# Performance work log

Measured on AMD Instinct MI355X. Metric: run time of the kernel, lower is better.

The kernel has to match this reference:

```python
import jax, jax.numpy as jnp
import numpy as np

D_HEAD = 64
MASK_FILL = -1000000.0


def setup_inputs() -> dict:
    key = jax.random.key(0)
    ks = jax.random.split(key, 5)
    batch, seq, d_model, n_heads, d_head = 4, 2048, 1024, 16, D_HEAD
    # xavier_uniform bound for [d_model, n_heads, d_head]: treated as fan_in=d_model, fan_out=n_heads*d_head
    bound_qkv = float(np.sqrt(6.0 / (d_model + n_heads * d_head)))
    bound_out = float(np.sqrt(6.0 / (d_head + n_heads * d_model)))
    return {
        "resid": jax.random.normal(ks[0], (batch, seq, d_model), dtype=jnp.float32),
        "W_Q": jax.random.uniform(ks[1], (d_model, n_heads, d_head), jnp.float32, -bound_qkv, bound_qkv),
        "W_K": jax.random.uniform(ks[2], (d_model, n_heads, d_head), jnp.float32, -bound_qkv, bound_qkv),
        "W_V": jax.random.uniform(ks[3], (d_model, n_heads, d_head), jnp.float32, -bound_qkv, bound_qkv),
        "W_out": jax.random.uniform(ks[4], (d_head, n_heads, d_model), jnp.float32, -bound_out, bound_out),
        "b_out": jnp.zeros((d_model,), dtype=jnp.float32),
    }


def reference(resid, W_Q, W_K, W_V, W_out, b_out):
    # resid: [b, s, d]; W_Q/K/V: [d, h, dh]; W_out: [dh, h, d]
    seq = resid.shape[1]
    d_head = W_Q.shape[-1]
    q = jnp.einsum('bsd,dhk->bshk', resid, W_Q)
    k = jnp.einsum('bsd,dhk->bshk', resid, W_K)
    v = jnp.einsum('bsd,dhk->bshk', resid, W_V)
    scores = jnp.einsum('bqhk,bkhd->bhqd', q, k.astype(q.dtype)) if False else jnp.einsum('bqhc,bshc->bhqs', q, k)
    scores = scores / jnp.sqrt(jnp.asarray(d_head, dtype=scores.dtype))
    causal_mask = jnp.triu(jnp.ones((seq, seq), dtype=bool), k=1)
    scores = jnp.where(causal_mask, MASK_FILL, scores)
    probs = jax.nn.softmax(scores, axis=-1)  # [b, h, q, s]
    z = jnp.einsum('bhqs,bshc->bqhc', probs, v)
    out = jnp.einsum('bqhc,chd->bqd', z, W_out) + b_out
    return out
```

## Files before the change

### kernel.cpp

```cpp
#include <hip/hip_runtime.h>
#include <hip/hip_bf16.h>


typedef short s16x8 __attribute__((ext_vector_type(8)));
typedef short s16x4 __attribute__((ext_vector_type(4)));
typedef float f32x4 __attribute__((ext_vector_type(4)));

#define MFMA_BF16(A, B, C) __builtin_amdgcn_mfma_f32_16x16x32_bf16((A), (B), (C), 0, 0, 0)

#if __has_builtin(__builtin_amdgcn_exp2f)
#define EXP2(x) __builtin_amdgcn_exp2f(x)
#else
#define EXP2(x) exp2f(x)
#endif
#if __has_builtin(__builtin_amdgcn_rcpf)
#define RCP(x) __builtin_amdgcn_rcpf(x)
#else
#define RCP(x) (1.0f / (x))
#endif

__device__ __forceinline__ short f2bf(float f) {
    __bf16 h = (__bf16)f;
    return __builtin_bit_cast(short, h);
}

__device__ __forceinline__ void gld16(const unsigned short* g, unsigned short* l) {
    __builtin_amdgcn_global_load_lds(
        (const __attribute__((address_space(1))) unsigned int*)g,
        (__attribute__((address_space(3))) unsigned int*)l, 16, 0, 0);
}

__global__ __launch_bounds__(256) void prep_fused(
    const float* __restrict__ resid, const float* __restrict__ WQ,
    const float* __restrict__ WK, const float* __restrict__ WV,
    const float* __restrict__ Wout,
    unsigned short* __restrict__ residb, unsigned short* __restrict__ Wqkvt,
    unsigned short* __restrict__ W2t)
{
    const int bid = blockIdx.x;
    if (bid < 8192) {
        const int i = bid * 256 + threadIdx.x;
        const float4 v = ((const float4*)resid)[i];
        s16x4 o;
        o[0] = f2bf(v.x); o[1] = f2bf(v.y); o[2] = f2bf(v.z); o[3] = f2bf(v.w);
        *(s16x4*)(residb + (size_t)i * 4) = o;
        return;
    }
    __shared__ unsigned short tile[64][66];
    const int id2 = bid - 8192;
    const int which = id2 >> 8;
    const int sub = id2 & 255;
    const int tx = threadIdx.x & 63, ty = threadIdx.x >> 6;
    if (which < 3) {
        const float* W = which == 0 ? WQ : (which == 1 ? WK : WV);
        unsigned short* Wt = Wqkvt + (size_t)which * 1024 * 1024;
        const int n0 = (sub & 15) * 64, k0 = (sub >> 4) * 64;
        #pragma unroll
        for (int i = ty; i < 64; i += 4)
            tile[i][tx] = (unsigned short)f2bf(W[(size_t)(k0 + i) * 1024 + n0 + tx]);
        __syncthreads();
        #pragma unroll
        for (int i = ty; i < 64; i += 4)
            Wt[(size_t)(n0 + i) * 1024 + k0 + tx] = tile[tx][i];
    } else {
        const int d0 = (sub & 15) * 64, h = sub >> 4;
        #pragma unroll
        for (int c = ty; c < 64; c += 4)
            tile[c][tx] = (unsigned short)f2bf(Wout[(size_t)(c * 16 + h) * 1024 + d0 + tx]);
        __syncthreads();
        #pragma unroll
        for (int i = ty; i < 64; i += 4)
            W2t[(size_t)(d0 + i) * 1024 + h * 64 + tx] = tile[tx][i];
    }
}

template <int MODE>
__global__ __launch_bounds__(256, 2) void gemm_bt(
    const unsigned short* __restrict__ A,
    const unsigned short* __restrict__ Bt,
    float* __restrict__ Cf, const float* __restrict__ bias,
    unsigned short* __restrict__ Qb, unsigned short* __restrict__ Kb,
    unsigned short* __restrict__ Vt,
    int M, int N, int K)
{
    __shared__ __align__(16) unsigned short AB[2 * 128 * 72];
    const int tid  = threadIdx.x;
    const int lane = tid & 63;
    const int w    = tid >> 6;
    const int wm   = w & 1, wn = w >> 1;
    const int quad = lane >> 4, fl = lane & 15;
    const int m0 = blockIdx.y * 128, n0 = blockIdx.x * 128;

    const unsigned short* gp[9];
    unsigned ldso[9];
    #pragma unroll
    for (int i = 0; i < 9; ++i) {
        const int c = i * 256 + tid;
        const int cm = c % 1152;
        const int r = cm / 9, cl0 = cm % 9;
        const int cl = (cl0 == 8) ? 0 : cl0;
        gp[i] = (c < 1152 ? A + (size_t)(m0 + r) * K : Bt + (size_t)(n0 + r) * K) + cl * 8;
        ldso[i] = (unsigned)c * 8u;
    }

    f32x4 acc[4][4];
    #pragma unroll
    for (int i = 0; i < 4; ++i)
        #pragma unroll
        for (int j = 0; j < 4; ++j)
            acc[i][j] = (f32x4){0.f, 0.f, 0.f, 0.f};

    for (int kt = 0; kt < K; kt += 64) {
        __syncthreads();
        #pragma unroll
        for (int i = 0; i < 9; ++i)
            gld16(gp[i] + kt, AB + ldso[i]);
        __syncthreads();
        #pragma unroll
        for (int ko = 0; ko < 2; ++ko) {
            s16x8 af[4], bf[4];
            #pragma unroll
            for (int mi = 0; mi < 4; ++mi)
                af[mi] = *(const s16x8*)(AB + (wm * 64 + mi * 16 + fl) * 72 + ko * 32 + quad * 8);
            #pragma unroll
            for (int ni = 0; ni < 4; ++ni)
                bf[ni] = *(const s16x8*)(AB + 9216 + (wn * 64 + ni * 16 + fl) * 72 + ko * 32 + quad * 8);
            #pragma unroll
            for (int mi = 0; mi < 4; ++mi)
                #pragma unroll
                for (int ni = 0; ni < 4; ++ni)
                    acc[mi][ni] = MFMA_BF16(af[mi], bf[ni], acc[mi][ni]);
        }
    }

    if (MODE == 0) {
        #pragma unroll
        for (int ni = 0; ni < 4; ++ni) {
            const int col = n0 + wn * 64 + ni * 16 + fl;
            const float bv = bias[col];
            #pragma unroll
            for (int mi = 0; mi < 4; ++mi) {
                const int row = m0 + wm * 64 + mi * 16 + quad * 4;
                #pragma unroll
                for (int r = 0; r < 4; ++r)
                    Cf[(size_t)(row + r) * N + col] = acc[mi][ni][r] + bv;
            }
        }
    } else {
        #pragma unroll
        for (int ni = 0; ni < 4; ++ni) {
            const int colg = n0 + wn * 64 + ni * 16 + fl;
            #pragma unroll
            for (int mi = 0; mi < 4; ++mi) {
                const int token = m0 + wm * 64 + mi * 16 + quad * 4;
                if (n0 < 1024) {
                    #pragma unroll
                    for (int r = 0; r < 4; ++r)
                        Qb[(size_t)(token + r) * 1024 + colg] = (unsigned short)f2bf(acc[mi][ni][r]);
                } else if (n0 < 2048) {
                    #pragma unroll
                    for (int r = 0; r < 4; ++r)
                        Kb[(size_t)(token + r) * 1024 + (colg - 1024)] = (unsigned short)f2bf(acc[mi][ni][r]);
                } else {
                    const int cc = colg - 2048;
                    const int hh = cc >> 6, cl = cc & 63;
                    const int bb = token >> 11, ss = token & 2047;
                    s16x4 pv;
                    pv[0] = f2bf(acc[mi][ni][0]); pv[1] = f2bf(acc[mi][ni][1]);
                    pv[2] = f2bf(acc[mi][ni][2]); pv[3] = f2bf(acc[mi][ni][3]);
                    *(s16x4*)(Vt + (size_t)((bb * 16 + hh) * 64 + cl) * 2048 + ss) = pv;
                }
            }
        }
    }
}

template <bool DIAG>
__device__ __forceinline__ void attn_tile(
    int s0, int wl, int wq0, int fl, int quad,
    const unsigned short* __restrict__ KV, const unsigned short* __restrict__ Vs,
    unsigned short* __restrict__ PbW,
    const s16x8 (&qfr)[2][2], f32x4 (&zt)[2][4], float (&ls)[2])
{
    const float SC = 0.18033688011112042f;
    const float M  = 32.0f;
    #pragma unroll
    for (int c4 = 0; c4 < 4; ++c4) {
        if (DIAG && c4 > wl) break;
        #pragma unroll
        for (int e = 0; e < 2; ++e) {
            const int f = 2 * c4 + e;
            const unsigned short* Krow = KV + (f * 16 + fl) * 72;
            const s16x8 kf0 = *(const s16x8*)(Krow + quad * 8);
            const s16x8 kf1 = *(const s16x8*)(Krow + 32 + quad * 8);
            #pragma unroll
            for (int g = 0; g < 2; ++g) {
                unsigned short* pw = PbW + (g * 16 + fl) * 36 + e * 16 + quad * 4;
                if (DIAG && f > 2 * wl + g) {
                    *(s16x4*)pw = (s16x4){0, 0, 0, 0};
                } else {
                    f32x4 z = (f32x4){0.f, 0.f, 0.f, 0.f};
                    z = MFMA_BF16(kf0, qfr[g][0], z);
                    z = MFMA_BF16(kf1, qfr[g][1], z);
                    float p[4];
                    #pragma unroll
                    for (int r = 0; r < 4; ++r) {
                        float arg = fmaf(z[r], SC, -M);
                        if (DIAG && f == 2 * wl + g) {
                            const int s = s0 + f * 16 + quad * 4 + r;
                            const int qi = wq0 + g * 16 + fl;
                            if (s > qi) arg = -100.f;
                        }
                        p[r] = EXP2(arg);
                    }
                    ls[g] += (p[0] + p[1]) + (p[2] + p[3]);
                    s16x4 pk;
                    pk[0] = f2bf(p[0]); pk[1] = f2bf(p[1]);
                    pk[2] = f2bf(p[2]); pk[3] = f2bf(p[3]);
                    *(s16x4*)pw = pk;
                }
            }
        }
        const s16x8 pf0 = *(const s16x8*)(PbW + fl * 36 + quad * 8);
        const s16x8 pf1 = *(const s16x8*)(PbW + (16 + fl) * 36 + quad * 8);
        #pragma unroll
        for (int mf = 0; mf < 4; ++mf) {
            const s16x8 vf = *(const s16x8*)(Vs + (mf * 16 + fl) * 136 + c4 * 32 + quad * 8);
            zt[0][mf] = MFMA_BF16(vf, pf0, zt[0][mf]);
            zt[1][mf] = MFMA_BF16(vf, pf1, zt[1][mf]);
        }
    }
}

__global__ __launch_bounds__(512, 4) void attn_causal(
    const unsigned short* __restrict__ Qb,
    const unsigned short* __restrict__ Kb,
    const unsigned short* __restrict__ Vt,
    unsigned short* __restrict__ Zb)
{
    __shared__ __align__(16) unsigned short KV[17920];
    __shared__ __align__(16) unsigned short Pb[8][32 * 36];
    const int tid = threadIdx.x, lane = tid & 63, w = tid >> 6;
    const int quad = lane >> 4, fl = lane & 15;
    const int lid = blockIdx.x;
    const int g8 = lid >> 6;
    const int qb = g8 < 4 ? 7 - g8 : g8 - 4;
    const int bh = lid & 63, b = bh >> 4, h = bh & 15;
    const int wq0 = qb * 256 + w * 32;
    const int wl = w & 3;
    const int dt = 2 * qb + (w >> 2);

    const unsigned short* Kbase = Kb + (size_t)b * 2048 * 1024 + h * 64;
    const unsigned short* Vbase = Vt + (size_t)bh * 64 * 2048;
    unsigned short* PbW = Pb[w];
    const unsigned short* Vs = KV + 9216;

    s16x8 qfr[2][2];
    #pragma unroll
    for (int g = 0; g < 2; ++g) {
        const unsigned short* Qrow = Qb + (size_t)(b * 2048 + wq0 + g * 16 + fl) * 1024 + h * 64;
        qfr[g][0] = *(const s16x8*)(Qrow + quad * 8);
        qfr[g][1] = *(const s16x8*)(Qrow + 32 + quad * 8);
    }

    const unsigned short* gsp[5];
    int sadv[5];
    unsigned ldsb[5];
    #pragma unroll
    for (int i = 0; i < 5; ++i) {
        const int W = w + 8 * i;
        if (W < 35) {
            const int c = W * 64 + lane;
            if (c < 1152) {
                const int r = c / 9, cl0 = c % 9;
                const int cl = (cl0 == 8) ? 0 : cl0;
                gsp[i] = Kbase + r * 1024 + cl * 8;  sadv[i] = 128 * 1024;
            } else {
                const int cc = c - 1152;
                const int r = cc / 17, cl0 = cc % 17;
                const int cl = (cl0 == 16) ? 0 : cl0;
                gsp[i] = Vbase + r * 2048 + cl * 8;  sadv[i] = 128;
            }
            ldsb[i] = (unsigned)c * 8u;
        }
    }

    f32x4 zt[2][4];
    #pragma unroll
    for (int g = 0; g < 2; ++g)
        #pragma unroll
        for (int mf = 0; mf < 4; ++mf) zt[g][mf] = (f32x4){0.f, 0.f, 0.f, 0.f};
    float ls[2] = {0.f, 0.f};
    const int ntiles = 2 * qb + 2;

    for (int kt = 0; kt < ntiles; ++kt) {
        __syncthreads();
        #pragma unroll
        for (int i = 0; i < 5; ++i)
            if (w + 8 * i < 35)
                gld16(gsp[i], KV + ldsb[i]);
        #pragma unroll
        for (int i = 0; i < 5; ++i)
            if (w + 8 * i < 35)
                gsp[i] += sadv[i];
        __syncthreads();

        if (kt < dt) {
            attn_tile<false>(kt << 7, wl, wq0, fl, quad, KV, Vs, PbW, qfr, zt, ls);
        } else if (kt == dt) {
            attn_tile<true>(kt << 7, wl, wq0, fl, quad, KV, Vs, PbW, qfr, zt, ls);
        }
    }
    #pragma unroll
    for (int g = 0; g < 2; ++g) {
        float lt = ls[g];
        lt += __shfl_xor(lt, 16);
        lt += __shfl_xor(lt, 32);
        const float inv = RCP(lt);
        unsigned short* Zrow = Zb + (size_t)(b * 2048 + wq0 + g * 16 + fl) * 1024 + h * 64;
        #pragma unroll
        for (int mf = 0; mf < 4; ++mf) {
            s16x4 o;
            o[0] = f2bf(zt[g][mf][0] * inv); o[1] = f2bf(zt[g][mf][1] * inv);
            o[2] = f2bf(zt[g][mf][2] * inv); o[3] = f2bf(zt[g][mf][3] * inv);
            *(s16x4*)(Zrow + mf * 16 + quad * 4) = o;
        }
    }
}

extern "C" void kernel_launch(void* const* d_in, const int* in_sizes, int n_in,
                              void* d_out, int out_size, void* d_ws, size_t ws_size,
                              hipStream_t stream) {
    const float* resid = (const float*)d_in[0];
    const float* WQ    = (const float*)d_in[1];
    const float* WK    = (const float*)d_in[2];
    const float* WV    = (const float*)d_in[3];
    const float* Wout  = (const float*)d_in[4];
    const float* bout  = (const float*)d_in[5];
    float* out = (float*)d_out;

    char* p = (char*)d_ws;
    auto alloc = [&](size_t bytes) { void* r = (void*)p; p += (bytes + 255) & ~(size_t)255; return r; };
    unsigned short* residb = (unsigned short*)alloc(8192ull * 1024 * 2);
    unsigned short* Wqkvt  = (unsigned short*)alloc(3072ull * 1024 * 2);
    unsigned short* W2t    = (unsigned short*)alloc(1024ull * 1024 * 2);
    unsigned short* Qbuf   = (unsigned short*)alloc(8192ull * 1024 * 2);
    unsigned short* Kbuf   = (unsigned short*)alloc(8192ull * 1024 * 2);
    unsigned short* Vtb    = (unsigned short*)alloc(64ull * 64 * 2048 * 2);
    unsigned short* Zbuf   = (unsigned short*)alloc(8192ull * 1024 * 2);

    prep_fused<<<9216, 256, 0, stream>>>(resid, WQ, WK, WV, Wout, residb, Wqkvt, W2t);
    gemm_bt<1><<<dim3(24, 64), 256, 0, stream>>>(residb, Wqkvt, nullptr, nullptr,
                                                 Qbuf, Kbuf, Vtb, 8192, 3072, 1024);
    attn_causal<<<512, 512, 0, stream>>>(Qbuf, Kbuf, Vtb, Zbuf);
    gemm_bt<0><<<dim3(8, 64), 256, 0, stream>>>(Zbuf, W2t, out, bout,
                                                nullptr, nullptr, nullptr, 8192, 1024, 1024);
}
```

Baseline: 261.5 us.

## Replace QKV projection GEMM with 256x256-tile, 8-wave pipelined kernel

Adds a dedicated QKV projection kernel using 256x256 output tiles with 512 threads, double-buffered 128 KB dynamic LDS loaded through direct global-to-LDS copies, XOR-swizzled layout, a grouped block-index swizzle for L2 locality, and interleaved barriers with raised priority around MFMA phases. The aim is more data reuse per loaded tile and better overlap of loads with matrix math than the previous 128-tile GEMM. In exchange it uses far more LDS per block, which limits occupancy, and it hardcodes the problem shape.

```diff
diff --git a/kernel.cpp b/kernel.cpp
--- a/kernel.cpp
+++ b/kernel.cpp
@@ -71,6 +71,161 @@
         #pragma unroll
         for (int i = ty; i < 64; i += 4)
             W2t[(size_t)(d0 + i) * 1024 + h * 64 + tx] = tile[tx][i];
+    }
+}
+
+__global__ __launch_bounds__(512, 2) void gemm256_qkv(
+    const unsigned short* __restrict__ A,
+    const unsigned short* __restrict__ Bt,
+    unsigned short* __restrict__ Qb, unsigned short* __restrict__ Kb,
+    unsigned short* __restrict__ Vt)
+{
+    extern __shared__ __align__(16) unsigned short S[];
+    constexpr int LDK = 1024, NT = 16;
+    const int tid = threadIdx.x, lane = tid & 63, w = tid >> 6;
+    const int wm = w >> 2, wn = w & 3;
+    const int quad = lane >> 4, fl = lane & 15;
+
+    const int wg  = blockIdx.x;
+    const int swz = (wg & 7) * 48 + (wg >> 3);
+    const int bx  = swz % 12, by = swz / 12;
+    const int m0  = by * 256, n0 = bx * 256;
+
+    const int srow = (tid >> 6) * 16 + (lane >> 2);
+    const int sswz = ((lane & 3) ^ ((lane >> 2) & 3)) * 8;
+    const unsigned short* pa[2];
+    const unsigned short* pb[2];
+    #pragma unroll
+    for (int j = 0; j < 2; ++j) {
+        pa[j] = A  + (size_t)(m0 + srow + j * 128) * LDK + sswz;
+        pb[j] = Bt + (size_t)(n0 + srow + j * 128) * LDK + sswz;
+    }
+    const int dst = tid * 8;
+
+    const int sxor = (quad ^ (fl & 3)) * 8;
+    const int aoff = (wm * 128 + fl) * 32 + sxor;
+    const int boff = 16384 + (wn * 64 + fl) * 32 + sxor;
+
+    f32x4 acc[8][4];
+    #pragma unroll
+    for (int m = 0; m < 8; ++m)
+        #pragma unroll
+        for (int n = 0; n < 4; ++n) acc[m][n] = (f32x4){0.f, 0.f, 0.f, 0.f};
+
+    gld16(pa[0], S + dst);
+    gld16(pa[1], S + 4096 + dst);
+    gld16(pb[0], S + 16384 + dst);
+    gld16(pb[1], S + 20480 + dst);
+    gld16(pa[0] + 32, S + 8192 + dst);
+    gld16(pa[1] + 32, S + 12288 + dst);
+    gld16(pb[0] + 32, S + 24576 + dst);
+    gld16(pb[1] + 32, S + 28672 + dst);
+
+    for (int t = 0; t < NT; ++t) {
+        const int cur = (t & 1) << 15;
+        unsigned short* Sn = S + (cur ^ 32768);
+        const unsigned short* Sc = S + cur;
+        const int know = (t + 1 < NT) ? (t + 1) * 64 : 0;
+
+        asm volatile("s_waitcnt vmcnt(4)" ::: "memory");
+        __builtin_amdgcn_s_barrier();
+
+        s16x8 bf[4], af[4];
+        #pragma unroll
+        for (int ni = 0; ni < 4; ++ni) bf[ni] = *(const s16x8*)(Sc + boff + ni * 512);
+        #pragma unroll
+        for (int mi = 0; mi < 4; ++mi) af[mi] = *(const s16x8*)(Sc + aoff + mi * 512);
+        gld16(pa[0] + know, Sn + dst);
+        gld16(pa[1] + know, Sn + 4096 + dst);
+        asm volatile("" ::: "memory");
+        __builtin_amdgcn_s_barrier();
+        __builtin_amdgcn_s_setprio(1);
+        #pragma unroll
+        for (int mi = 0; mi < 4; ++mi)
+            #pragma unroll
+            for (int ni = 0; ni < 4; ++ni)
+                acc[mi][ni] = MFMA_BF16(af[mi], bf[ni], acc[mi][ni]);
+        __builtin_amdgcn_s_setprio(0);
+        asm volatile("" ::: "memory");
+        __builtin_amdgcn_s_barrier();
+        #pragma unroll
+        for (int mi = 0; mi < 4; ++mi) af[mi] = *(const s16x8*)(Sc + aoff + (4 + mi) * 512);
+        gld16(pb[0] + know, Sn + 16384 + dst);
+        gld16(pb[1] + know, Sn + 20480 + dst);
+        asm volatile("" ::: "memory");
+        __builtin_amdgcn_s_barrier();
+        __builtin_amdgcn_s_setprio(1);
+        #pragma unroll
+        for (int mi = 0; mi < 4; ++mi)
+            #pragma unroll
+            for (int ni = 0; ni < 4; ++ni)
+                acc[4 + mi][ni] = MFMA_BF16(af[mi], bf[ni], acc[4 + mi][ni]);
+        __builtin_amdgcn_s_setprio(0);
+
+        asm volatile("s_waitcnt vmcnt(4)" ::: "memory");
+        __builtin_amdgcn_s_barrier();
+        #pragma unroll
+        for (int ni = 0; ni < 4; ++ni) bf[ni] = *(const s16x8*)(Sc + 8192 + boff + ni * 512);
+        #pragma unroll
+        for (int mi = 0; mi < 4; ++mi) af[mi] = *(const s16x8*)(Sc + 8192 + aoff + mi * 512);
+        gld16(pa[0] + know + 32, Sn + 8192 + dst);
+        gld16(pa[1] + know + 32, Sn + 12288 + dst);
+        asm volatile("" ::: "memory");
+        __builtin_amdgcn_s_barrier();
+        __builtin_amdgcn_s_setprio(1);
+        #pragma unroll
+        for (int mi = 0; mi < 4; ++mi)
+            #pragma unroll
+            for (int ni = 0; ni < 4; ++ni)
+                acc[mi][ni] = MFMA_BF16(af[mi], bf[ni], acc[mi][ni]);
+        __builtin_amdgcn_s_setprio(0);
+        asm volatile("" ::: "memory");
+        __builtin_amdgcn_s_barrier();
+        #pragma unroll
+        for (int mi = 0; mi < 4; ++mi) af[mi] = *(const s16x8*)(Sc + 8192 + aoff + (4 + mi) * 512);
+        gld16(pb[0] + know + 32, Sn + 24576 + dst);
+        gld16(pb[1] + know + 32, Sn + 28672 + dst);
+        asm volatile("" ::: "memory");
+        __builtin_amdgcn_s_barrier();
+        __builtin_amdgcn_s_setprio(1);
+        #pragma unroll
+        for (int mi = 0; mi < 4; ++mi)
+            #pragma unroll
+            for (int ni = 0; ni < 4; ++ni)
+                acc[4 + mi][ni] = MFMA_BF16(af[mi], bf[ni], acc[4 + mi][ni]);
+        __builtin_amdgcn_s_setprio(0);
+    }
+
+    const int which = n0 >> 10;
+    if (which < 2) {
+        unsigned short* O = which == 0 ? Qb : Kb;
+        const int cbase = (n0 & 1023) + wn * 64;
+        #pragma unroll
+        for (int m = 0; m < 8; ++m) {
+            const int row = m0 + wm * 128 + m * 16 + quad * 4;
+            #pragma unroll
+            for (int ni = 0; ni < 4; ++ni) {
+                const int col = cbase + ni * 16 + fl;
+                #pragma unroll
+                for (int r = 0; r < 4; ++r)
+                    O[(size_t)(row + r) * 1024 + col] = (unsigned short)f2bf(acc[m][ni][r]);
+            }
+        }
+    } else {
+        const int hh = ((n0 - 2048) >> 6) + wn;
+        #pragma unroll
+        for (int m = 0; m < 8; ++m) {
+            const int token = m0 + wm * 128 + m * 16 + quad * 4;
+            const int bb = token >> 11, ss = token & 2047;
+            #pragma unroll
+            for (int ni = 0; ni < 4; ++ni) {
+                const int cl = ni * 16 + fl;
+                s16x4 pv;
+                pv[0] = f2bf(acc[m][ni][0]); pv[1] = f2bf(acc[m][ni][1]);
+                pv[2] = f2bf(acc[m][ni][2]); pv[3] = f2bf(acc[m][ni][3]);
+                *(s16x4*)(Vt + (size_t)((bb * 16 + hh) * 64 + cl) * 2048 + ss) = pv;
+            }
+        }
     }
 }
 
@@ -349,9 +504,15 @@
     unsigned short* Vtb    = (unsigned short*)alloc(64ull * 64 * 2048 * 2);
     unsigned short* Zbuf   = (unsigned short*)alloc(8192ull * 1024 * 2);
 
+    static bool s_attr = false;
+    if (!s_attr) {
+        hipFuncSetAttribute(reinterpret_cast<const void*>(gemm256_qkv),
+                            hipFuncAttributeMaxDynamicSharedMemorySize, 131072);
+        s_attr = true;
+    }
+
     prep_fused<<<9216, 256, 0, stream>>>(resid, WQ, WK, WV, Wout, residb, Wqkvt, W2t);
-    gemm_bt<1><<<dim3(24, 64), 256, 0, stream>>>(residb, Wqkvt, nullptr, nullptr,
-                                                 Qbuf, Kbuf, Vtb, 8192, 3072, 1024);
+    gemm256_qkv<<<384, 512, 131072, stream>>>(residb, Wqkvt, Qbuf, Kbuf, Vtb);
     attn_causal<<<512, 512, 0, stream>>>(Qbuf, Kbuf, Vtb, Zbuf);
     gemm_bt<0><<<dim3(8, 64), 256, 0, stream>>>(Zbuf, W2t, out, bout,
                                                 nullptr, nullptr, nullptr, 8192, 1024, 1024);
```

After: 277.1 us. 5.9% more time.

## Add dedicated QKV GEMM kernel with async LDS loads, swizzle and double buffering

Applied to the files above, without the earlier changes.

Replaces the generic QKV projection GEMM with a dedicated 128x256-tile, 512-thread kernel. It uses direct global-to-LDS loads (gld16) into an XOR-swizzled, double-buffered shared memory layout, split-phase waitcnt/barrier pipelining, s_setprio around the MFMA bursts, and a workgroup index swizzle for L2 locality. The aim is to hide global load latency and cut LDS bank conflicts in the largest GEMM. In exchange it needs 96KB of dynamic LDS set via a function attribute, which may limit occupancy, and the hand-written wait counts are fragile.

```diff
diff --git a/kernel.cpp b/kernel.cpp
--- a/kernel.cpp
+++ b/kernel.cpp
@@ -74,13 +74,137 @@
     }
 }
 
+__global__ __launch_bounds__(512, 2) void gemm_qkv(
+    const unsigned short* __restrict__ A,
+    const unsigned short* __restrict__ Bt,
+    unsigned short* __restrict__ Qb, unsigned short* __restrict__ Kb,
+    unsigned short* __restrict__ Vt)
+{
+    extern __shared__ __align__(16) unsigned short S[];
+    constexpr int LDK = 1024, NT = 16;
+    const int tid = threadIdx.x, lane = tid & 63, w = tid >> 6;
+    const int wm = w >> 2, wn = w & 3;
+    const int quad = lane >> 4, fl = lane & 15;
+
+    const int wg  = blockIdx.x;
+    const int swz = (wg & 7) * 96 + (wg >> 3);
+    const int bx  = swz % 12, by = swz / 12;
+    const int m0  = by * 128, n0 = bx * 256;
+
+    const int srow = tid >> 2;
+    const int sk   = ((tid & 3) ^ ((tid >> 3) & 3)) * 8;
+    const unsigned short* pa  = A  + (size_t)(m0 + srow) * LDK + sk;
+    const unsigned short* pb0 = Bt + (size_t)(n0 + srow) * LDK + sk;
+    const unsigned short* pb1 = Bt + (size_t)(n0 + 128 + srow) * LDK + sk;
+    const int dst = tid * 8;
+
+    const int sx   = (quad ^ ((fl >> 1) & 3)) * 8;
+    const int arow = (wm * 64 + fl) * 32 + sx;
+    const int brow = 8192 + (wn * 64 + fl) * 32 + sx;
+
+    f32x4 acc[4][4];
+    #pragma unroll
+    for (int m = 0; m < 4; ++m)
+        #pragma unroll
+        for (int n = 0; n < 4; ++n) acc[m][n] = (f32x4){0.f, 0.f, 0.f, 0.f};
+
+    gld16(pa,       S + dst);
+    gld16(pb0,      S + 8192 + dst);
+    gld16(pb1,      S + 12288 + dst);
+    gld16(pa + 32,  S + 4096 + dst);
+    gld16(pb0 + 32, S + 16384 + dst);
+    gld16(pb1 + 32, S + 20480 + dst);
+
+    for (int t = 0; t < NT; ++t) {
+        unsigned short* Sc = S + (t & 1) * 24576;
+        unsigned short* Sn = S + ((t & 1) ^ 1) * 24576;
+        const int ka = (t + 1) * 64;
+        const bool pf = (t + 1 < NT);
+
+        asm volatile("s_waitcnt vmcnt(3)" ::: "memory");
+        __builtin_amdgcn_s_barrier();
+
+        s16x8 af[4], bfr[4];
+        #pragma unroll
+        for (int mi = 0; mi < 4; ++mi) af[mi]  = *(const s16x8*)(Sc + arow + mi * 512);
+        #pragma unroll
+        for (int ni = 0; ni < 4; ++ni) bfr[ni] = *(const s16x8*)(Sc + brow + ni * 512);
+        if (pf) {
+            gld16(pa + ka,  Sn + dst);
+            gld16(pb0 + ka, Sn + 8192 + dst);
+            gld16(pb1 + ka, Sn + 12288 + dst);
+        }
+        asm volatile("" ::: "memory");
+        __builtin_amdgcn_s_barrier();
+        __builtin_amdgcn_s_setprio(1);
+        #pragma unroll
+        for (int mi = 0; mi < 4; ++mi)
+            #pragma unroll
+            for (int ni = 0; ni < 4; ++ni)
+                acc[mi][ni] = MFMA_BF16(af[mi], bfr[ni], acc[mi][ni]);
+        __builtin_amdgcn_s_setprio(0);
+
+        if (pf) asm volatile("s_waitcnt vmcnt(3)" ::: "memory");
+        else    asm volatile("s_waitcnt vmcnt(0)" ::: "memory");
+        __builtin_amdgcn_s_barrier();
+        #pragma unroll
+        for (int mi = 0; mi < 4; ++mi) af[mi]  = *(const s16x8*)(Sc + 4096 + arow + mi * 512);
+        #pragma unroll
+        for (int ni = 0; ni < 4; ++ni) bfr[ni] = *(const s16x8*)(Sc + 8192 + brow + ni * 512);
+        if (pf) {
+            gld16(pa + ka + 32,  Sn + 4096 + dst);
+            gld16(pb0 + ka + 32, Sn + 16384 + dst);
+            gld16(pb1 + ka + 32, Sn + 20480 + dst);
+        }
+        asm volatile("" ::: "memory");
+        __builtin_amdgcn_s_barrier();
+        __builtin_amdgcn_s_setprio(1);
+        #pragma unroll
+        for (int mi = 0; mi < 4; ++mi)
+            #pragma unroll
+            for (int ni = 0; ni < 4; ++ni)
+                acc[mi][ni] = MFMA_BF16(af[mi], bfr[ni], acc[mi][ni]);
+        __builtin_amdgcn_s_setprio(0);
+    }
+
+    const int which = n0 >> 10;
+    if (which < 2) {
+        unsigned short* O = which == 0 ? Qb : Kb;
+        const int cbase = (n0 & 1023) + wn * 64;
+        #pragma unroll
+        for (int mi = 0; mi < 4; ++mi) {
+            const int row = m0 + wm * 64 + mi * 16 + quad * 4;
+            #pragma unroll
+            for (int ni = 0; ni < 4; ++ni) {
+                const int col = cbase + ni * 16 + fl;
+                #pragma unroll
+                for (int r = 0; r < 4; ++r)
+                    O[(size_t)(row + r) * 1024 + col] = (unsigned short)f2bf(acc[mi][ni][r]);
+            }
+        }
+    } else {
+        const int hh = ((n0 - 2048) >> 6) + wn;
+        #pragma unroll
+        for (int mi = 0; mi < 4; ++mi) {
+            const int token = m0 + wm * 64 + mi * 16 + quad * 4;
+            const int bb = token >> 11, ss = token & 2047;
+            #pragma unroll
+            for (int ni = 0; ni < 4; ++ni) {
+                const int cl = ni * 16 + fl;
+                s16x4 pv;
+                pv[0] = f2bf(acc[mi][ni][0]); pv[1] = f2bf(acc[mi][ni][1]);
+                pv[2] = f2bf(acc[mi][ni][2]); pv[3] = f2bf(acc[mi][ni][3]);
+                *(s16x4*)(Vt + (size_t)((bb * 16 + hh) * 64 + cl) * 2048 + ss) = pv;
+            }
+        }
+    }
+}
+
 template <int MODE>
 __global__ __launch_bounds__(256, 2) void gemm_bt(
     const unsigned short* __restrict__ A,
     const unsigned short* __restrict__ Bt,
     float* __restrict__ Cf, const float* __restrict__ bias,
-    unsigned short* __restrict__ Qb, unsigned short* __restrict__ Kb,
-    unsigned short* __restrict__ Vt,
     int M, int N, int K)
 {
     __shared__ __align__(16) unsigned short AB[2 * 128 * 72];
@@ -133,44 +257,16 @@
         }
     }
 
-    if (MODE == 0) {
-        #pragma unroll
-        for (int ni = 0; ni < 4; ++ni) {
-            const int col = n0 + wn * 64 + ni * 16 + fl;
-            const float bv = bias[col];
-            #pragma unroll
-            for (int mi = 0; mi < 4; ++mi) {
-                const int row = m0 + wm * 64 + mi * 16 + quad * 4;
-                #pragma unroll
-                for (int r = 0; r < 4; ++r)
-                    Cf[(size_t)(row + r) * N + col] = acc[mi][ni][r] + bv;
-            }
-        }
-    } else {
-        #pragma unroll
-        for (int ni = 0; ni < 4; ++ni) {
-            const int colg = n0 + wn * 64 + ni * 16 + fl;
-            #pragma unroll
-            for (int mi = 0; mi < 4; ++mi) {
-                const int token = m0 + wm * 64 + mi * 16 + quad * 4;
-                if (n0 < 1024) {
-                    #pragma unroll
-                    for (int r = 0; r < 4; ++r)
-                        Qb[(size_t)(token + r) * 1024 + colg] = (unsigned short)f2bf(acc[mi][ni][r]);
-                } else if (n0 < 2048) {
-                    #pragma unroll
-                    for (int r = 0; r < 4; ++r)
-                        Kb[(size_t)(token + r) * 1024 + (colg - 1024)] = (unsigned short)f2bf(acc[mi][ni][r]);
-                } else {
-                    const int cc = colg - 2048;
-                    const int hh = cc >> 6, cl = cc & 63;
-                    const int bb = token >> 11, ss = token & 2047;
-                    s16x4 pv;
-                    pv[0] = f2bf(acc[mi][ni][0]); pv[1] = f2bf(acc[mi][ni][1]);
-                    pv[2] = f2bf(acc[mi][ni][2]); pv[3] = f2bf(acc[mi][ni][3]);
-                    *(s16x4*)(Vt + (size_t)((bb * 16 + hh) * 64 + cl) * 2048 + ss) = pv;
-                }
-            }
+    #pragma unroll
+    for (int ni = 0; ni < 4; ++ni) {
+        const int col = n0 + wn * 64 + ni * 16 + fl;
+        const float bv = bias[col];
+        #pragma unroll
+        for (int mi = 0; mi < 4; ++mi) {
+            const int row = m0 + wm * 64 + mi * 16 + quad * 4;
+            #pragma unroll
+            for (int r = 0; r < 4; ++r)
+                Cf[(size_t)(row + r) * N + col] = acc[mi][ni][r] + bv;
         }
     }
 }
@@ -349,10 +445,15 @@
     unsigned short* Vtb    = (unsigned short*)alloc(64ull * 64 * 2048 * 2);
     unsigned short* Zbuf   = (unsigned short*)alloc(8192ull * 1024 * 2);
 
+    static bool s_attr = false;
+    if (!s_attr) {
+        hipFuncSetAttribute(reinterpret_cast<const void*>(gemm_qkv),
+                            hipFuncAttributeMaxDynamicSharedMemorySize, 98304);
+        s_attr = true;
+    }
+
     prep_fused<<<9216, 256, 0, stream>>>(resid, WQ, WK, WV, Wout, residb, Wqkvt, W2t);
-    gemm_bt<1><<<dim3(24, 64), 256, 0, stream>>>(residb, Wqkvt, nullptr, nullptr,
-                                                 Qbuf, Kbuf, Vtb, 8192, 3072, 1024);
+    gemm_qkv<<<768, 512, 98304, stream>>>(residb, Wqkvt, Qbuf, Kbuf, Vtb);
     attn_causal<<<512, 512, 0, stream>>>(Qbuf, Kbuf, Vtb, Zbuf);
-    gemm_bt<0><<<dim3(8, 64), 256, 0, stream>>>(Zbuf, W2t, out, bout,
-                                                nullptr, nullptr, nullptr, 8192, 1024, 1024);
-}
+    gemm_bt<0><<<dim3(8, 64), 256, 0, stream>>>(Zbuf, W2t, out, bout, 8192, 1024, 1024);
+}
```

After: 263.5 us. About the same (+0.8%).
